# Performance work log

Measured on AMD Instinct MI355X. Metric: run time of the kernel, lower is better.

The kernel has to match this reference:

```python
import jax, jax.numpy as jnp
import numpy as np

B, S, D = 64, 512, 512  # bias broadcast and final bmm force S == input_dim == dim_v
DK, DV = 512, 512


def setup_inputs() -> dict:
    key = jax.random.key(0)
    ks = jax.random.split(key, 16)
    sc = 0.02
    inp = {
        "sent_emb": jax.random.normal(ks[0], (B, S, D), jnp.float32),
        "pos_emb": jax.random.normal(ks[1], (B, S, D), jnp.float32),
        "branch_emb": jax.random.normal(ks[2], (B, S, D), jnp.float32),
        # Linear weights stored torch-style: [out, in]
        "Wq": jax.random.normal(ks[3], (DK, D), jnp.float32) * sc,
        "bq": jnp.zeros((DK,), jnp.float32),
        "Wk": jax.random.normal(ks[4], (DK, D), jnp.float32) * sc,
        "bk": jnp.zeros((DK,), jnp.float32),
        "Wv": jax.random.normal(ks[5], (DV, D), jnp.float32) * sc,
        "bv": jnp.zeros((DV,), jnp.float32),
        "Wpq": jax.random.normal(ks[6], (D, D), jnp.float32) * sc,
        "bpq": jnp.zeros((D,), jnp.float32),
        "Wpk": jax.random.normal(ks[7], (D, D), jnp.float32) * sc,
        "bpk": jnp.zeros((D,), jnp.float32),
        "bias": jax.random.normal(ks[8], (D,), jnp.float32) * sc,
    }
    return inp


def reference(sent_emb, pos_emb, branch_emb, Wq, bq, Wk, bk, Wv, bv, Wpq, bpq, Wpk, bpk, bias):
    d = sent_emb.shape[-1]
    norm = 1.0 / jnp.sqrt(jnp.asarray(2.0 * d, sent_emb.dtype))
    # projections (torch Linear: x @ W.T + b)
    Q = sent_emb @ Wq.T + bq          # [B,S,DK]
    K = sent_emb @ Wk.T + bk          # [B,S,DK]
    V = sent_emb @ Wv.T + bv          # [B,S,DV]
    Uq = pos_emb @ Wpq.T + bpq        # [B,S,D]
    Uk = pos_emb @ Wpk.T + bpk        # [B,S,D]
    text_score = jnp.einsum('bsd,btd->bst', Q, K) * norm   # [B,S,S]
    pos_score = jnp.einsum('bsd,btd->bst', Uq, Uk) * norm  # [B,S,S]
    att = text_score + pos_score + bias                    # bias [D] broadcasts over last axis (S==D)
    att_softmax = jax.nn.softmax(att, axis=2)
    # torch.bmm(att, V.permute(0,2,1)): out[b,i,j] = sum_t att[b,i,t] * V[b,j,t]
    output = jnp.einsum('bit,bjt->bij', att_softmax, V)    # [B,S,S] (DV==S)
    return (att_softmax, output)
```

## Files before the change

kernel.cpp:

```cpp
#include <hip/hip_runtime.h>

typedef unsigned short u16;
typedef unsigned int   u32;
typedef __bf16 bf16x8 __attribute__((ext_vector_type(8)));
typedef float  f32x4  __attribute__((ext_vector_type(4)));

#define BATCH 64
#define SEQ   512
#define BSS   (64 * 512 * 512)
#define MTOT  (64 * 512)

__device__ __forceinline__ u16 f2bf(float f) {
  u32 u = __builtin_bit_cast(u32, f);
  u += 0x7FFFu + ((u >> 16) & 1u);
  return (u16)(u >> 16);
}

__device__ __forceinline__ void gl16(const void* g, void* l) {
  __builtin_amdgcn_global_load_lds(
      (__attribute__((address_space(1))) void*)g,
      (__attribute__((address_space(3))) void*)l,
      16, 0, 0);
}

__global__ __launch_bounds__(256) void cvt_bf16_kernel(
    const float* __restrict__ in, u16* __restrict__ out, int n8) {
  int i = blockIdx.x * 256 + threadIdx.x;
  if (i >= n8) return;
  const float4* p = reinterpret_cast<const float4*>(in) + (size_t)i * 2;
  float4 x = p[0], y = p[1];
  uint4 r;
  r.x = (u32)f2bf(x.x) | ((u32)f2bf(x.y) << 16);
  r.y = (u32)f2bf(x.z) | ((u32)f2bf(x.w) << 16);
  r.z = (u32)f2bf(y.x) | ((u32)f2bf(y.y) << 16);
  r.w = (u32)f2bf(y.z) | ((u32)f2bf(y.w) << 16);
  reinterpret_cast<uint4*>(out)[i] = r;
}

__global__ __launch_bounds__(256) void pack_w_kernel(
    const float* __restrict__ wq, const float* __restrict__ wk,
    const float* __restrict__ wv, const float* __restrict__ wpq,
    const float* __restrict__ wpk, u16* __restrict__ wc1, u16* __restrict__ wc2) {
  int i = blockIdx.x * 256 + threadIdx.x;
  int which = i >> 18;
  int off = i & 262143;
  const float* src = which == 0 ? wq : which == 1 ? wk : which == 2 ? wv
                   : which == 3 ? wpq : wpk;
  u16 h = f2bf(src[off]);
  if (which < 3) wc1[(size_t)which * 262144 + off] = h;
  else           wc2[(size_t)(which - 3) * 262144 + off] = h;
}

__global__ __launch_bounds__(256) void pack_bias_kernel(
    const float* __restrict__ bq, const float* __restrict__ bk,
    const float* __restrict__ bv, const float* __restrict__ bpq,
    const float* __restrict__ bpk, float* __restrict__ b1, float* __restrict__ b2) {
  int i = blockIdx.x * 256 + threadIdx.x;
  if (i < 1536) {
    b1[i] = i < 512 ? bq[i] : i < 1024 ? bk[i - 512] : bv[i - 1024];
  } else {
    int j = i - 1536;
    b2[j] = j < 512 ? bpq[j] : bpk[j - 512];
  }
}

template <int MODE>
__global__ __launch_bounds__(256) void gemm_nt(
    const u16* __restrict__ A, const u16* __restrict__ Bm, int K,
    unsigned long sAz, unsigned long sBz,
    u16* __restrict__ U0, u16* __restrict__ U1, u16* __restrict__ U2,
    float* __restrict__ F, unsigned long sFz,
    const float* __restrict__ bias, float scale) {
  __shared__ u16 lsA[128 * 32];
  __shared__ u16 lsB[128 * 32];

  const int t = threadIdx.x;
  const int z = blockIdx.z;
  const int m0 = blockIdx.y * 128;
  const int n0 = blockIdx.x * 128;
  A += (size_t)z * sAz;
  Bm += (size_t)z * sBz;
  if (MODE >= 2) F += (size_t)z * sFz;

  const int srow = t >> 2;
  const int scol = (t & 3) * 8;
  const u16* gA0 = A + (size_t)(m0 + srow) * K + scol;
  const u16* gB0 = Bm + (size_t)(n0 + srow) * K + scol;
  const size_t rowskip = (size_t)64 * K;
  u16* lA0 = lsA + t * 8;
  u16* lA1 = lsA + 2048 + t * 8;
  u16* lB0 = lsB + t * 8;
  u16* lB1 = lsB + 2048 + t * 8;

  const int l = t & 63;
  const int w = t >> 6;
  const int wm = (w & 1) * 64;
  const int wn = (w >> 1) * 64;
  const int fr = l & 15;
  const int fk = (l >> 4) * 8;

  f32x4 acc[4][4];
#pragma unroll
  for (int i = 0; i < 4; ++i)
#pragma unroll
    for (int j = 0; j < 4; ++j) acc[i][j] = (f32x4){0.f, 0.f, 0.f, 0.f};

  for (int k0 = 0; k0 < K; k0 += 32) {
    gl16(gA0 + k0, lA0);
    gl16(gA0 + rowskip + k0, lA1);
    gl16(gB0 + k0, lB0);
    gl16(gB0 + rowskip + k0, lB1);
    __syncthreads();
    bf16x8 af[4], bfg[4];
#pragma unroll
    for (int mt = 0; mt < 4; ++mt)
      af[mt] = *reinterpret_cast<const bf16x8*>(&lsA[(wm + mt * 16 + fr) * 32 + fk]);
#pragma unroll
    for (int nt = 0; nt < 4; ++nt)
      bfg[nt] = *reinterpret_cast<const bf16x8*>(&lsB[(wn + nt * 16 + fr) * 32 + fk]);
#pragma unroll
    for (int mt = 0; mt < 4; ++mt)
#pragma unroll
      for (int nt = 0; nt < 4; ++nt)
        acc[mt][nt] = __builtin_amdgcn_mfma_f32_16x16x32_bf16(
            af[mt], bfg[nt], acc[mt][nt], 0, 0, 0);
    __syncthreads();
  }

  const int cr = (l >> 4) * 4;
  const int cc = l & 15;
#pragma unroll
  for (int mt = 0; mt < 4; ++mt) {
#pragma unroll
    for (int nt = 0; nt < 4; ++nt) {
      const int col = n0 + wn + nt * 16 + cc;
#pragma unroll
      for (int r = 0; r < 4; ++r) {
        const int row = m0 + wm + mt * 16 + cr + r;
        float v = acc[mt][nt][r];
        if (MODE == 0) {
          v += bias[col];
          u16 h = f2bf(v);
          const int which = col >> 9, c = col & 511;
          if (which == 0)      U0[(size_t)row * 1024 + c] = h;
          else if (which == 1) U1[(size_t)row * 1024 + c] = h;
          else                 U2[(size_t)row * 512 + c] = h;
        } else if (MODE == 1) {
          v += bias[col];
          u16 h = f2bf(v);
          const int which = col >> 9, c = col & 511;
          if (which == 0) U0[(size_t)row * 1024 + 512 + c] = h;
          else            U1[(size_t)row * 1024 + 512 + c] = h;
        } else if (MODE == 2) {
          F[(size_t)row * 512 + col] = v * scale + bias[col];
        } else {
          F[(size_t)row * 512 + col] = v;
        }
      }
    }
  }
}

__global__ __launch_bounds__(256) void softmax_kernel(
    const float* __restrict__ logits, float* __restrict__ attF,
    u16* __restrict__ attB) {
  const int row = blockIdx.x * 4 + (threadIdx.x >> 6);
  const int l = threadIdx.x & 63;
  const float* p = logits + (size_t)row * 512 + l * 8;
  float4 a = *reinterpret_cast<const float4*>(p);
  float4 b = *reinterpret_cast<const float4*>(p + 4);
  float v[8] = {a.x, a.y, a.z, a.w, b.x, b.y, b.z, b.w};
  float mx = v[0];
#pragma unroll
  for (int j = 1; j < 8; ++j) mx = fmaxf(mx, v[j]);
#pragma unroll
  for (int s = 32; s > 0; s >>= 1) mx = fmaxf(mx, __shfl_xor(mx, s, 64));
  float sum = 0.f;
#pragma unroll
  for (int j = 0; j < 8; ++j) {
    v[j] = __expf(v[j] - mx);
    sum += v[j];
  }
#pragma unroll
  for (int s = 32; s > 0; s >>= 1) sum += __shfl_xor(sum, s, 64);
  const float inv = 1.0f / sum;
#pragma unroll
  for (int j = 0; j < 8; ++j) v[j] *= inv;
  float* o = attF + (size_t)row * 512 + l * 8;
  float4 oa = {v[0], v[1], v[2], v[3]};
  float4 ob = {v[4], v[5], v[6], v[7]};
  *reinterpret_cast<float4*>(o) = oa;
  *reinterpret_cast<float4*>(o + 4) = ob;
  uint4 r;
  r.x = (u32)f2bf(v[0]) | ((u32)f2bf(v[1]) << 16);
  r.y = (u32)f2bf(v[2]) | ((u32)f2bf(v[3]) << 16);
  r.z = (u32)f2bf(v[4]) | ((u32)f2bf(v[5]) << 16);
  r.w = (u32)f2bf(v[6]) | ((u32)f2bf(v[7]) << 16);
  *reinterpret_cast<uint4*>(attB + (size_t)row * 512 + l * 8) = r;
}

extern "C" void kernel_launch(void* const* d_in, const int* in_sizes, int n_in,
                              void* d_out, int out_size, void* d_ws,
                              size_t ws_size, hipStream_t stream) {
  const float* sent = (const float*)d_in[0];
  const float* pos  = (const float*)d_in[1];
  const float* Wq  = (const float*)d_in[3];
  const float* bq  = (const float*)d_in[4];
  const float* Wk  = (const float*)d_in[5];
  const float* bk  = (const float*)d_in[6];
  const float* Wv  = (const float*)d_in[7];
  const float* bv  = (const float*)d_in[8];
  const float* Wpq = (const float*)d_in[9];
  const float* bpq = (const float*)d_in[10];
  const float* Wpk = (const float*)d_in[11];
  const float* bpk = (const float*)d_in[12];
  const float* abias = (const float*)d_in[13];
  float* out = (float*)d_out;

  char* ws = (char*)d_ws;
  u16* Xs   = (u16*)(ws);
  u16* Xp   = (u16*)(ws + 33554432ul);
  u16* QU   = (u16*)(ws + 67108864ul);
  u16* KU   = (u16*)(ws + 134217728ul);
  u16* Vb   = (u16*)(ws + 201326592ul);
  u16* attB = (u16*)(ws + 234881024ul);
  u16* Wc1  = (u16*)(ws + 268435456ul);
  u16* Wc2  = (u16*)(ws + 270008320ul);
  float* b1 = (float*)(ws + 271056896ul);
  float* b2 = (float*)(ws + 271063040ul);

  float* attF   = out;
  float* out2   = out + BSS;
  float* logits = out + BSS;

  cvt_bf16_kernel<<<8192, 256, 0, stream>>>(sent, Xs, MTOT * 512 / 8);
  cvt_bf16_kernel<<<8192, 256, 0, stream>>>(pos, Xp, MTOT * 512 / 8);
  pack_w_kernel<<<5120, 256, 0, stream>>>(Wq, Wk, Wv, Wpq, Wpk, Wc1, Wc2);
  pack_bias_kernel<<<10, 256, 0, stream>>>(bq, bk, bv, bpq, bpk, b1, b2);

  gemm_nt<0><<<dim3(12, 256, 1), 256, 0, stream>>>(
      Xs, Wc1, 512, 0ul, 0ul, QU, KU, Vb, nullptr, 0ul, b1, 1.0f);
  gemm_nt<1><<<dim3(8, 256, 1), 256, 0, stream>>>(
      Xp, Wc2, 512, 0ul, 0ul, QU, KU, nullptr, nullptr, 0ul, b2, 1.0f);

  gemm_nt<2><<<dim3(4, 4, BATCH), 256, 0, stream>>>(
      QU, KU, 1024, (unsigned long)SEQ * 1024, (unsigned long)SEQ * 1024,
      nullptr, nullptr, nullptr, logits, (unsigned long)SEQ * SEQ, abias,
      0.03125f);

  softmax_kernel<<<8192, 256, 0, stream>>>(logits, attF, attB);

  gemm_nt<3><<<dim3(4, 4, BATCH), 256, 0, stream>>>(
      attB, Vb, 512, (unsigned long)SEQ * SEQ, (unsigned long)SEQ * SEQ,
      nullptr, nullptr, nullptr, out2, (unsigned long)SEQ * SEQ, nullptr, 1.0f);

  (void)in_sizes; (void)n_in; (void)out_size; (void)ws_size;
}
```

Baseline: 587.6 us.

## Fuse score GEMM, softmax, and PV GEMM into one attention kernel

Replaces the separate logits GEMM, softmax kernel, and attention-times-V GEMM with one kernel. Each 512-thread block computes a full 64x512 score tile in registers, does the row softmax with cross-wave LDS reductions, writes the fp32 probabilities, and feeds bf16 probabilities through LDS into the PV MFMA loop. This removes the fp32 logits round trip and the bf16 attention buffer in global memory. It also merges the two input conversion launches into one. In exchange the fused kernel has a large register footprint, no double buffering, only 512 blocks, and a serialized per-wave staging of P.

```diff
diff --git a/kernel.cpp b/kernel.cpp
--- a/kernel.cpp
+++ b/kernel.cpp
@@ -23,10 +23,13 @@
       16, 0, 0);
 }
 
-__global__ __launch_bounds__(256) void cvt_bf16_kernel(
-    const float* __restrict__ in, u16* __restrict__ out, int n8) {
+__global__ __launch_bounds__(256) void cvt2_bf16_kernel(
+    const float* __restrict__ in0, u16* __restrict__ out0,
+    const float* __restrict__ in1, u16* __restrict__ out1, int n8) {
   int i = blockIdx.x * 256 + threadIdx.x;
-  if (i >= n8) return;
+  const float* in = in0;
+  u16* out = out0;
+  if (i >= n8) { i -= n8; in = in1; out = out1; }
   const float4* p = reinterpret_cast<const float4*>(in) + (size_t)i * 2;
   float4 x = p[0], y = p[1];
   uint4 r;
@@ -67,20 +70,14 @@
 template <int MODE>
 __global__ __launch_bounds__(256) void gemm_nt(
     const u16* __restrict__ A, const u16* __restrict__ Bm, int K,
-    unsigned long sAz, unsigned long sBz,
     u16* __restrict__ U0, u16* __restrict__ U1, u16* __restrict__ U2,
-    float* __restrict__ F, unsigned long sFz,
-    const float* __restrict__ bias, float scale) {
+    const float* __restrict__ bias) {
   __shared__ u16 lsA[128 * 32];
   __shared__ u16 lsB[128 * 32];
 
   const int t = threadIdx.x;
-  const int z = blockIdx.z;
   const int m0 = blockIdx.y * 128;
   const int n0 = blockIdx.x * 128;
-  A += (size_t)z * sAz;
-  Bm += (size_t)z * sBz;
-  if (MODE >= 2) F += (size_t)z * sFz;
 
   const int srow = t >> 2;
   const int scol = (t & 3) * 8;
@@ -137,66 +134,216 @@
 #pragma unroll
       for (int r = 0; r < 4; ++r) {
         const int row = m0 + wm + mt * 16 + cr + r;
-        float v = acc[mt][nt][r];
+        float v = acc[mt][nt][r] + bias[col];
+        u16 h = f2bf(v);
+        const int which = col >> 9, c = col & 511;
         if (MODE == 0) {
-          v += bias[col];
-          u16 h = f2bf(v);
-          const int which = col >> 9, c = col & 511;
           if (which == 0)      U0[(size_t)row * 1024 + c] = h;
           else if (which == 1) U1[(size_t)row * 1024 + c] = h;
           else                 U2[(size_t)row * 512 + c] = h;
-        } else if (MODE == 1) {
-          v += bias[col];
-          u16 h = f2bf(v);
-          const int which = col >> 9, c = col & 511;
+        } else {
           if (which == 0) U0[(size_t)row * 1024 + 512 + c] = h;
           else            U1[(size_t)row * 1024 + 512 + c] = h;
-        } else if (MODE == 2) {
-          F[(size_t)row * 512 + col] = v * scale + bias[col];
-        } else {
-          F[(size_t)row * 512 + col] = v;
         }
       }
     }
   }
 }
 
-__global__ __launch_bounds__(256) void softmax_kernel(
-    const float* __restrict__ logits, float* __restrict__ attF,
-    u16* __restrict__ attB) {
-  const int row = blockIdx.x * 4 + (threadIdx.x >> 6);
-  const int l = threadIdx.x & 63;
-  const float* p = logits + (size_t)row * 512 + l * 8;
-  float4 a = *reinterpret_cast<const float4*>(p);
-  float4 b = *reinterpret_cast<const float4*>(p + 4);
-  float v[8] = {a.x, a.y, a.z, a.w, b.x, b.y, b.z, b.w};
-  float mx = v[0];
-#pragma unroll
-  for (int j = 1; j < 8; ++j) mx = fmaxf(mx, v[j]);
-#pragma unroll
-  for (int s = 32; s > 0; s >>= 1) mx = fmaxf(mx, __shfl_xor(mx, s, 64));
-  float sum = 0.f;
-#pragma unroll
-  for (int j = 0; j < 8; ++j) {
-    v[j] = __expf(v[j] - mx);
-    sum += v[j];
-  }
-#pragma unroll
-  for (int s = 32; s > 0; s >>= 1) sum += __shfl_xor(sum, s, 64);
-  const float inv = 1.0f / sum;
-#pragma unroll
-  for (int j = 0; j < 8; ++j) v[j] *= inv;
-  float* o = attF + (size_t)row * 512 + l * 8;
-  float4 oa = {v[0], v[1], v[2], v[3]};
-  float4 ob = {v[4], v[5], v[6], v[7]};
-  *reinterpret_cast<float4*>(o) = oa;
-  *reinterpret_cast<float4*>(o + 4) = ob;
-  uint4 r;
-  r.x = (u32)f2bf(v[0]) | ((u32)f2bf(v[1]) << 16);
-  r.y = (u32)f2bf(v[2]) | ((u32)f2bf(v[3]) << 16);
-  r.z = (u32)f2bf(v[4]) | ((u32)f2bf(v[5]) << 16);
-  r.w = (u32)f2bf(v[6]) | ((u32)f2bf(v[7]) << 16);
-  *reinterpret_cast<uint4*>(attB + (size_t)row * 512 + l * 8) = r;
+__global__ __launch_bounds__(512, 2) void fused_attn(
+    const u16* __restrict__ QU, const u16* __restrict__ KU,
+    const u16* __restrict__ Vb, const float* __restrict__ bias,
+    float* __restrict__ attF, float* __restrict__ outO) {
+  __shared__ u16 lsA[64 * 32];
+  __shared__ u16 lsB[512 * 32];
+  __shared__ u16 lsP[64 * 40];
+  __shared__ float sred[64 * 8];
+
+  const int t = threadIdx.x;
+  const int b = blockIdx.x;
+  const int rg = blockIdx.y;
+  const int l = t & 63;
+  const int w = t >> 6;
+  const int wn = w * 64;
+  const int fr = l & 15;
+  const int fk = (l >> 4) * 8;
+  const int q = l >> 4;
+  const int cc = l & 15;
+  const int cr = q * 4;
+
+  const u16* Aq = QU + ((size_t)(b * 512 + rg * 64)) * 1024;
+  const u16* Bk = KU + ((size_t)b * 512) * 1024;
+
+  const u16* gA = Aq + (size_t)(t >> 2) * 1024 + (t & 3) * 8;
+  const u16* gB = Bk + (size_t)(t >> 2) * 1024 + (t & 3) * 8;
+
+  float bc[4];
+#pragma unroll
+  for (int nt = 0; nt < 4; ++nt) bc[nt] = bias[wn + nt * 16 + cc];
+
+  f32x4 acc[4][4];
+#pragma unroll
+  for (int i = 0; i < 4; ++i)
+#pragma unroll
+    for (int j = 0; j < 4; ++j) acc[i][j] = (f32x4){0.f, 0.f, 0.f, 0.f};
+
+  for (int k0 = 0; k0 < 1024; k0 += 32) {
+    __syncthreads();
+    if (t < 256) gl16(gA + k0, lsA + t * 8);
+#pragma unroll
+    for (int qq = 0; qq < 4; ++qq)
+      gl16(gB + (size_t)qq * 128 * 1024 + k0, lsB + (qq * 512 + t) * 8);
+    __syncthreads();
+    bf16x8 af[4], bfg[4];
+#pragma unroll
+    for (int mt = 0; mt < 4; ++mt)
+      af[mt] = *reinterpret_cast<const bf16x8*>(&lsA[(mt * 16 + fr) * 32 + fk]);
+#pragma unroll
+    for (int nt = 0; nt < 4; ++nt)
+      bfg[nt] = *reinterpret_cast<const bf16x8*>(&lsB[(wn + nt * 16 + fr) * 32 + fk]);
+#pragma unroll
+    for (int mt = 0; mt < 4; ++mt)
+#pragma unroll
+      for (int nt = 0; nt < 4; ++nt)
+        acc[mt][nt] = __builtin_amdgcn_mfma_f32_16x16x32_bf16(
+            af[mt], bfg[nt], acc[mt][nt], 0, 0, 0);
+  }
+
+#pragma unroll
+  for (int mt = 0; mt < 4; ++mt)
+#pragma unroll
+    for (int nt = 0; nt < 4; ++nt)
+#pragma unroll
+      for (int r = 0; r < 4; ++r)
+        acc[mt][nt][r] = acc[mt][nt][r] * 0.03125f + bc[nt];
+
+  float pm[4][4];
+#pragma unroll
+  for (int mt = 0; mt < 4; ++mt)
+#pragma unroll
+    for (int r = 0; r < 4; ++r) {
+      float m = fmaxf(fmaxf(acc[mt][0][r], acc[mt][1][r]),
+                      fmaxf(acc[mt][2][r], acc[mt][3][r]));
+#pragma unroll
+      for (int s = 1; s < 16; s <<= 1) m = fmaxf(m, __shfl_xor(m, s, 64));
+      pm[mt][r] = m;
+    }
+  if (cc == 0) {
+#pragma unroll
+    for (int mt = 0; mt < 4; ++mt)
+#pragma unroll
+      for (int r = 0; r < 4; ++r)
+        sred[(mt * 16 + cr + r) * 8 + w] = pm[mt][r];
+  }
+  __syncthreads();
+  float rowm[4][4];
+#pragma unroll
+  for (int mt = 0; mt < 4; ++mt)
+#pragma unroll
+    for (int r = 0; r < 4; ++r) {
+      const float* p = &sred[(mt * 16 + cr + r) * 8];
+      f32x4 a = *reinterpret_cast<const f32x4*>(p);
+      f32x4 c = *reinterpret_cast<const f32x4*>(p + 4);
+      rowm[mt][r] = fmaxf(fmaxf(fmaxf(a[0], a[1]), fmaxf(a[2], a[3])),
+                          fmaxf(fmaxf(c[0], c[1]), fmaxf(c[2], c[3])));
+    }
+  __syncthreads();
+
+#pragma unroll
+  for (int mt = 0; mt < 4; ++mt)
+#pragma unroll
+    for (int r = 0; r < 4; ++r) {
+      float s = 0.f;
+#pragma unroll
+      for (int nt = 0; nt < 4; ++nt) {
+        float e = __expf(acc[mt][nt][r] - rowm[mt][r]);
+        acc[mt][nt][r] = e;
+        s += e;
+      }
+#pragma unroll
+      for (int sh = 1; sh < 16; sh <<= 1) s += __shfl_xor(s, sh, 64);
+      pm[mt][r] = s;
+    }
+  if (cc == 0) {
+#pragma unroll
+    for (int mt = 0; mt < 4; ++mt)
+#pragma unroll
+      for (int r = 0; r < 4; ++r)
+        sred[(mt * 16 + cr + r) * 8 + w] = pm[mt][r];
+  }
+  __syncthreads();
+#pragma unroll
+  for (int mt = 0; mt < 4; ++mt)
+#pragma unroll
+    for (int r = 0; r < 4; ++r) {
+      const float* p = &sred[(mt * 16 + cr + r) * 8];
+      f32x4 a = *reinterpret_cast<const f32x4*>(p);
+      f32x4 c = *reinterpret_cast<const f32x4*>(p + 4);
+      float s = (a[0] + a[1]) + (a[2] + a[3]) + (c[0] + c[1]) + (c[2] + c[3]);
+      rowm[mt][r] = 1.0f / s;
+    }
+
+  float* attBase = attF + (size_t)b * 262144 + (size_t)rg * 64 * 512;
+#pragma unroll
+  for (int mt = 0; mt < 4; ++mt)
+#pragma unroll
+    for (int nt = 0; nt < 4; ++nt)
+#pragma unroll
+      for (int r = 0; r < 4; ++r) {
+        float a = acc[mt][nt][r] * rowm[mt][r];
+        acc[mt][nt][r] = a;
+        attBase[(size_t)(mt * 16 + cr + r) * 512 + wn + nt * 16 + cc] = a;
+      }
+
+  f32x4 acc2[4][4];
+#pragma unroll
+  for (int i = 0; i < 4; ++i)
+#pragma unroll
+    for (int j = 0; j < 4; ++j) acc2[i][j] = (f32x4){0.f, 0.f, 0.f, 0.f};
+
+  const u16* gV = Vb + (size_t)b * 262144 + (size_t)(t >> 2) * 512 + (t & 3) * 8;
+
+  for (int ts = 0; ts < 16; ++ts) {
+    __syncthreads();
+#pragma unroll
+    for (int qq = 0; qq < 4; ++qq)
+      gl16(gV + (size_t)qq * 128 * 512 + ts * 32, lsB + (qq * 512 + t) * 8);
+    if (w == (ts >> 1)) {
+      const int h0 = (ts & 1) * 2;
+#pragma unroll
+      for (int mt = 0; mt < 4; ++mt)
+#pragma unroll
+        for (int hh = 0; hh < 2; ++hh)
+#pragma unroll
+          for (int r = 0; r < 4; ++r)
+            lsP[(mt * 16 + cr + r) * 40 + hh * 16 + cc] =
+                f2bf(acc[mt][h0 + hh][r]);
+    }
+    __syncthreads();
+    bf16x8 pa[4], vbf[4];
+#pragma unroll
+    for (int mt = 0; mt < 4; ++mt)
+      pa[mt] = *reinterpret_cast<const bf16x8*>(&lsP[(mt * 16 + fr) * 40 + fk]);
+#pragma unroll
+    for (int nt = 0; nt < 4; ++nt)
+      vbf[nt] = *reinterpret_cast<const bf16x8*>(&lsB[(wn + nt * 16 + fr) * 32 + fk]);
+#pragma unroll
+    for (int mt = 0; mt < 4; ++mt)
+#pragma unroll
+      for (int nt = 0; nt < 4; ++nt)
+        acc2[mt][nt] = __builtin_amdgcn_mfma_f32_16x16x32_bf16(
+            pa[mt], vbf[nt], acc2[mt][nt], 0, 0, 0);
+  }
+
+  float* oBase = outO + (size_t)b * 262144 + (size_t)rg * 64 * 512;
+#pragma unroll
+  for (int mt = 0; mt < 4; ++mt)
+#pragma unroll
+    for (int nt = 0; nt < 4; ++nt)
+#pragma unroll
+      for (int r = 0; r < 4; ++r)
+        oBase[(size_t)(mt * 16 + cr + r) * 512 + wn + nt * 16 + cc] =
+            acc2[mt][nt][r];
 }
 
 extern "C" void kernel_launch(void* const* d_in, const int* in_sizes, int n_in,
@@ -223,36 +370,22 @@
   u16* QU   = (u16*)(ws + 67108864ul);
   u16* KU   = (u16*)(ws + 134217728ul);
   u16* Vb   = (u16*)(ws + 201326592ul);
-  u16* attB = (u16*)(ws + 234881024ul);
   u16* Wc1  = (u16*)(ws + 268435456ul);
   u16* Wc2  = (u16*)(ws + 270008320ul);
   float* b1 = (float*)(ws + 271056896ul);
   float* b2 = (float*)(ws + 271063040ul);
 
-  float* attF   = out;
-  float* out2   = out + BSS;
-  float* logits = out + BSS;
-
-  cvt_bf16_kernel<<<8192, 256, 0, stream>>>(sent, Xs, MTOT * 512 / 8);
-  cvt_bf16_kernel<<<8192, 256, 0, stream>>>(pos, Xp, MTOT * 512 / 8);
+  float* attF = out;
+  float* out2 = out + BSS;
+
+  cvt2_bf16_kernel<<<16384, 256, 0, stream>>>(sent, Xs, pos, Xp, MTOT * 512 / 8);
   pack_w_kernel<<<5120, 256, 0, stream>>>(Wq, Wk, Wv, Wpq, Wpk, Wc1, Wc2);
   pack_bias_kernel<<<10, 256, 0, stream>>>(bq, bk, bv, bpq, bpk, b1, b2);
 
-  gemm_nt<0><<<dim3(12, 256, 1), 256, 0, stream>>>(
-      Xs, Wc1, 512, 0ul, 0ul, QU, KU, Vb, nullptr, 0ul, b1, 1.0f);
-  gemm_nt<1><<<dim3(8, 256, 1), 256, 0, stream>>>(
-      Xp, Wc2, 512, 0ul, 0ul, QU, KU, nullptr, nullptr, 0ul, b2, 1.0f);
-
-  gemm_nt<2><<<dim3(4, 4, BATCH), 256, 0, stream>>>(
-      QU, KU, 1024, (unsigned long)SEQ * 1024, (unsigned long)SEQ * 1024,
-      nullptr, nullptr, nullptr, logits, (unsigned long)SEQ * SEQ, abias,
-      0.03125f);
-
-  softmax_kernel<<<8192, 256, 0, stream>>>(logits, attF, attB);
-
-  gemm_nt<3><<<dim3(4, 4, BATCH), 256, 0, stream>>>(
-      attB, Vb, 512, (unsigned long)SEQ * SEQ, (unsigned long)SEQ * SEQ,
-      nullptr, nullptr, nullptr, out2, (unsigned long)SEQ * SEQ, nullptr, 1.0f);
+  gemm_nt<0><<<dim3(12, 256, 1), 256, 0, stream>>>(Xs, Wc1, 512, QU, KU, Vb, b1);
+  gemm_nt<1><<<dim3(8, 256, 1), 256, 0, stream>>>(Xp, Wc2, 512, QU, KU, nullptr, b2);
+
+  fused_attn<<<dim3(BATCH, 8, 1), 512, 0, stream>>>(QU, KU, Vb, abias, attF, out2);
 
   (void)in_sizes; (void)n_in; (void)out_size; (void)ws_size;
 }
```

Result: slower. 992.6 us (+68.9%).
